# Kernel tuning notes

Hardware: AMD Instinct MI355X
Metric: run time of the kernel (lower is better)

Reference implementation:

```python
import jax, jax.numpy as jnp
import numpy as np

B, N, C, H = 1, 4096, 512, 8
S = 64  # sqrt(N), static


def setup_inputs() -> dict:
    key = jax.random.key(0)
    ks = jax.random.split(key, 4)
    d = C // H
    return {
        "x": jax.random.normal(ks[0], (B, N, C), dtype=jnp.float32),
        "num_heads": H,
        "bias": jnp.zeros((1,), dtype=jnp.float32),  # unused in original forward
        "scale": jnp.asarray(d ** -0.5, dtype=jnp.float32),
        "Wqkv": jax.random.normal(ks[1], (3 * C, C), dtype=jnp.float32) * (C ** -0.5),
        "bqkv": jnp.zeros((3 * C,), dtype=jnp.float32),
        "Wproj": jax.random.normal(ks[2], (C, C), dtype=jnp.float32) * (C ** -0.5),
        "bproj": jnp.zeros((C,), dtype=jnp.float32),
    }


def reference(x, num_heads, bias, scale, Wqkv, bqkv, Wproj, bproj):
    b, n, c = x.shape
    d = c // num_heads
    # fused QKV projection: [b, n, 3c] -> [3, b, h, n, d]
    qkv = (x @ Wqkv.T + bqkv).reshape(b, n, 3, num_heads, d).transpose(2, 0, 3, 1, 4)
    q, k, v = qkv[0] * scale, qkv[1], qkv[2]
    attn = jax.nn.softmax(jnp.einsum("bhnd,bhmd->bhnm", q, k), axis=-1)
    out = jnp.einsum("bhnm,bhmd->bhnd", attn, v)
    out = out.transpose(0, 2, 1, 3).reshape(b, n, c)
    out = out @ Wproj.T + bproj
    return out.reshape(b, S, S, c)
```

## Files before the change

kernel.cpp:

```cpp
#include <hip/hip_runtime.h>
#include <stdint.h>

#define NTOK 4096
#define CDIM 512
#define HEADS 8
#define DHEAD 64
#define PHEAD (NTOK * DHEAD)

typedef __bf16 bf16x8 __attribute__((ext_vector_type(8)));
typedef float f32x4 __attribute__((ext_vector_type(4)));

__device__ __forceinline__ unsigned short bfbits(float f) {
    return __builtin_bit_cast(unsigned short, (__bf16)f);
}

__device__ __forceinline__ f32x4 mfma32(bf16x8 a, bf16x8 b, f32x4 c) {
    return __builtin_amdgcn_mfma_f32_16x16x32_bf16(a, b, c, 0, 0, 0);
}

__device__ __forceinline__ void stage8(unsigned short* dst, const float* src) {
    const float4 v0 = *(const float4*)src;
    const float4 v1 = *(const float4*)(src + 4);
    ushort4 o0, o1;
    o0.x = bfbits(v0.x); o0.y = bfbits(v0.y); o0.z = bfbits(v0.z); o0.w = bfbits(v0.w);
    o1.x = bfbits(v1.x); o1.y = bfbits(v1.y); o1.z = bfbits(v1.z); o1.w = bfbits(v1.w);
    *(ushort4*)dst = o0;
    *(ushort4*)(dst + 4) = o1;
}

__global__ __launch_bounds__(256) void gemm_qkv(
    const float* __restrict__ A,
    const float* __restrict__ Bm,
    const float* __restrict__ bias,
    const float* __restrict__ scale_p,
    unsigned short* __restrict__ qkv_out)
{
    __shared__ __align__(16) unsigned short smem[64 * 136];
    unsigned short* lA = smem;
    unsigned short* lB = smem + 2048;

    const int tid = threadIdx.x;
    const int mBase = blockIdx.y * 64, nBase = blockIdx.x * 128;
    const int lane = tid & 63;
    const int w = __builtin_amdgcn_readfirstlane(tid >> 6);
    const int l16 = lane & 15, quad = lane >> 4;
    const int srow = tid >> 2, scol = (tid & 3) * 8;

    f32x4 acc[4][2] = {};

    for (int kt = 0; kt < CDIM; kt += 32) {
        __syncthreads();
        stage8(&lA[srow * 32 + scol], &A[(size_t)(mBase + srow) * CDIM + kt + scol]);
#pragma unroll
        for (int p = 0; p < 2; ++p) {
            const int r = p * 64 + srow;
            stage8(&lB[r * 32 + scol], &Bm[(size_t)(nBase + r) * CDIM + kt + scol]);
        }
        __syncthreads();

        bf16x8 af[4], bfr[2];
#pragma unroll
        for (int i = 0; i < 4; ++i)
            af[i] = *(const bf16x8*)&lA[(i * 16 + l16) * 32 + quad * 8];
#pragma unroll
        for (int j = 0; j < 2; ++j)
            bfr[j] = *(const bf16x8*)&lB[(w * 32 + j * 16 + l16) * 32 + quad * 8];
#pragma unroll
        for (int i = 0; i < 4; ++i)
#pragma unroll
            for (int j = 0; j < 2; ++j)
                acc[i][j] = mfma32(af[i], bfr[j], acc[i][j]);
    }

    const int three = nBase >> 9;
    const float scl = scale_p[0] * 1.44269504f;
    const float mul = (three == 0) ? scl : 1.0f;

    __syncthreads();
#pragma unroll
    for (int i = 0; i < 4; ++i)
#pragma unroll
        for (int j = 0; j < 2; ++j)
#pragma unroll
            for (int r = 0; r < 4; ++r) {
                const int rl = i * 16 + quad * 4 + r;
                const int cl = w * 32 + j * 16 + l16;
                const float v = (acc[i][j][r] + bias[nBase + cl]) * mul;
                smem[rl * 136 + cl] = bfbits(v);
            }
    __syncthreads();

    const size_t base3 = (size_t)three * (PHEAD * HEADS);
    if (three < 2) {
#pragma unroll
        for (int pass = 0; pass < 4; ++pass) {
            const int idx = pass * 256 + tid;
            const int rl16 = idx & 15, qc = (idx >> 4) & 7;
            const int hsel = (idx >> 7) & 1, t16l = (idx >> 8) & 3;
            const uint4 d = *(const uint4*)&smem[(t16l * 16 + rl16) * 136 + hsel * 64 + qc * 8];
            const int hh = ((nBase >> 6) + hsel) & 7;
            const int t16 = (mBase >> 4) + t16l;
            const size_t dst = base3 + (size_t)hh * PHEAD +
                (size_t)(((t16 * 2 + (qc >> 2)) * 64 + (qc & 3) * 16 + rl16) * 8);
            *(uint4*)&qkv_out[dst] = d;
        }
    } else {
#pragma unroll
        for (int pass = 0; pass < 4; ++pass) {
            const int idx = pass * 256 + tid;
            const int l16t = idx & 15, quadt = (idx >> 4) & 3;
            const int dt = (idx >> 6) & 3, k32l = (idx >> 8) & 1, hsel = (idx >> 9) & 1;
            const int col = hsel * 64 + dt * 16 + l16t;
            unsigned short o8[8];
#pragma unroll
            for (int e = 0; e < 4; ++e) {
                o8[e]     = smem[(k32l * 32 + quadt * 4 + e) * 136 + col];
                o8[e + 4] = smem[(k32l * 32 + 16 + quadt * 4 + e) * 136 + col];
            }
            const int hh = ((nBase >> 6) + hsel) & 7;
            const int k32 = (mBase >> 5) + k32l;
            const size_t dst = base3 + (size_t)hh * PHEAD +
                (size_t)(((k32 * 4 + dt) * 64 + quadt * 16 + l16t) * 8);
            *(uint4*)&qkv_out[dst] = *(uint4*)o8;
        }
    }
}

__global__ __launch_bounds__(256, 4) void flash6_k(
    const unsigned short* __restrict__ qf,
    const unsigned short* __restrict__ kf,
    const unsigned short* __restrict__ vf,
    unsigned short* __restrict__ attn_out)
{
    __shared__ float ldsO[4][32][68];
    __shared__ float sml[4][32];

    const int tid = threadIdx.x;
    const int lane = tid & 63;
    const int w = __builtin_amdgcn_readfirstlane(tid >> 6);
    const int l16 = lane & 15, quad = lane >> 4;
    const int h = blockIdx.x, qb = blockIdx.y;

    const unsigned short* qh = qf + (size_t)h * PHEAD;
    const unsigned short* kb = kf + (size_t)h * PHEAD + w * 65536;
    const unsigned short* vb = vf + (size_t)h * PHEAD + w * 65536;

    bf16x8 qfr[2][2];
#pragma unroll
    for (int qt = 0; qt < 2; ++qt)
#pragma unroll
        for (int d2 = 0; d2 < 2; ++d2)
            qfr[qt][d2] = *(const bf16x8*)&qh[((qb * 2 + qt) * 2 + d2) * 512 + lane * 8];

    bf16x8 ones;
#pragma unroll
    for (int j = 0; j < 8; ++j) ones[j] = (__bf16)1.0f;

    f32x4 oacc[4][2] = {};
    f32x4 lacc[2] = {};

    bf16x8 kA[4], kB[4];
#pragma unroll
    for (int i = 0; i < 4; ++i)
        kA[i] = *(const bf16x8*)&kb[i * 512 + lane * 8];

    auto body = [&](int g, bf16x8* kuse, bf16x8* kload) {
#pragma unroll
        for (int i = 0; i < 4; ++i)
            kload[i] = *(const bf16x8*)&kb[(g + 1) * 2048 + i * 512 + lane * 8];
        bf16x8 vc[4];
#pragma unroll
        for (int i = 0; i < 4; ++i)
            vc[i] = *(const bf16x8*)&vb[g * 2048 + i * 512 + lane * 8];

        f32x4 s[2][2];
#pragma unroll
        for (int kt = 0; kt < 2; ++kt)
#pragma unroll
            for (int qt = 0; qt < 2; ++qt) {
                f32x4 a = {};
                a = mfma32(kuse[kt * 2 + 0], qfr[qt][0], a);
                a = mfma32(kuse[kt * 2 + 1], qfr[qt][1], a);
                s[kt][qt] = a;
            }

        bf16x8 pf[2];
#pragma unroll
        for (int qt = 0; qt < 2; ++qt) {
            bf16x8 pb;
#pragma unroll
            for (int kt = 0; kt < 2; ++kt)
#pragma unroll
                for (int r = 0; r < 4; ++r)
                    pb[kt * 4 + r] = (__bf16)__builtin_amdgcn_exp2f(s[kt][qt][r]);
            pf[qt] = pb;
            lacc[qt] = mfma32(ones, pb, lacc[qt]);
        }
#pragma unroll
        for (int dt = 0; dt < 4; ++dt)
#pragma unroll
            for (int qt = 0; qt < 2; ++qt)
                oacc[dt][qt] = mfma32(vc[dt], pf[qt], oacc[dt][qt]);
    };

    for (int it = 0; it < 16; ++it) {
        body(it * 2 + 0, kA, kB);
        body(it * 2 + 1, kB, kA);
    }

    if (quad == 0) {
#pragma unroll
        for (int qt = 0; qt < 2; ++qt) sml[w][qt * 16 + l16] = lacc[qt][0];
    }
    __syncthreads();
#pragma unroll
    for (int qt = 0; qt < 2; ++qt) {
        const int q = qt * 16 + l16;
#pragma unroll
        for (int dt = 0; dt < 4; ++dt)
            *(f32x4*)&ldsO[w][q][dt * 16 + quad * 4] = oacc[dt][qt];
    }
    __syncthreads();
    {
        const int q = tid >> 3, dseg = (tid & 7) * 8;
        const float L = sml[0][q] + sml[1][q] + sml[2][q] + sml[3][q];
        const float inv = 1.f / L;
        unsigned short o8[8];
#pragma unroll
        for (int i = 0; i < 8; ++i) {
            const float v = ldsO[0][q][dseg + i] + ldsO[1][q][dseg + i] +
                            ldsO[2][q][dseg + i] + ldsO[3][q][dseg + i];
            o8[i] = bfbits(v * inv);
        }
        *(uint4*)&attn_out[(size_t)(qb * 32 + q) * CDIM + h * DHEAD + dseg] = *(uint4*)o8;
    }
}

__global__ __launch_bounds__(256) void gemm_proj(
    const unsigned short* __restrict__ A,
    const float* __restrict__ Bm,
    const float* __restrict__ bias,
    float* __restrict__ c_out)
{
    __shared__ __align__(16) unsigned short smem[2 * 64 * 32];
    unsigned short* lA = smem;
    unsigned short* lB = smem + 2048;

    const int tid = threadIdx.x;
    const int mBase = blockIdx.y * 64, nBase = blockIdx.x * 64;
    const int lane = tid & 63;
    const int w = __builtin_amdgcn_readfirstlane(tid >> 6);
    const int l16 = lane & 15, quad = lane >> 4;
    const int srow = tid >> 2, scol = (tid & 3) * 8;

    f32x4 acc[4] = {};

    for (int kt = 0; kt < CDIM; kt += 32) {
        __syncthreads();
        *(uint4*)&lA[srow * 32 + scol] =
            *(const uint4*)&A[(size_t)(mBase + srow) * CDIM + kt + scol];
        stage8(&lB[srow * 32 + scol], &Bm[(size_t)(nBase + srow) * CDIM + kt + scol]);
        __syncthreads();

        bf16x8 af[4], bfr;
#pragma unroll
        for (int i = 0; i < 4; ++i)
            af[i] = *(const bf16x8*)&lA[(i * 16 + l16) * 32 + quad * 8];
        bfr = *(const bf16x8*)&lB[(w * 16 + l16) * 32 + quad * 8];
#pragma unroll
        for (int i = 0; i < 4; ++i)
            acc[i] = mfma32(af[i], bfr, acc[i]);
    }

#pragma unroll
    for (int i = 0; i < 4; ++i)
#pragma unroll
        for (int r = 0; r < 4; ++r) {
            const int grow = mBase + i * 16 + quad * 4 + r;
            const int gcol = nBase + w * 16 + l16;
            c_out[(size_t)grow * CDIM + gcol] = acc[i][r] + bias[gcol];
        }
}

extern "C" void kernel_launch(void* const* d_in, const int* in_sizes, int n_in,
                              void* d_out, int out_size, void* d_ws, size_t ws_size,
                              hipStream_t stream) {
    const float* x       = (const float*)d_in[0];
    const float* scale_p = (const float*)d_in[3];
    const float* Wqkv    = (const float*)d_in[4];
    const float* bqkv    = (const float*)d_in[5];
    const float* Wproj   = (const float*)d_in[6];
    const float* bproj   = (const float*)d_in[7];
    float* out = (float*)d_out;

    char* ws = (char*)d_ws;
    const size_t OFF_QKV  = 0;
    const size_t OFF_ATTN = 12582912;
    const size_t NEEDED   = OFF_ATTN + 4194304;
    if (ws_size < NEEDED) return;

    unsigned short* qkvb  = (unsigned short*)(ws + OFF_QKV);
    unsigned short* attnb = (unsigned short*)(ws + OFF_ATTN);

    gemm_qkv<<<dim3(12, 64), 256, 0, stream>>>(x, Wqkv, bqkv, scale_p, qkvb);

    const unsigned short* qfr = qkvb;
    const unsigned short* kfr = qkvb + (size_t)PHEAD * HEADS;
    const unsigned short* vfr = qkvb + (size_t)2 * PHEAD * HEADS;
    flash6_k<<<dim3(8, 128), 256, 0, stream>>>(qfr, kfr, vfr, attnb);

    gemm_proj<<<dim3(8, 64), 256, 0, stream>>>(attnb, Wproj, bproj, out);
}
```

Baseline: 139.7 us.

## Split attention over key halves and merge partial outputs in projection GEMM

Adds a new attention kernel in which each block handles 64 queries against one half of the keys, instead of 32 queries against all keys. The four waves each take a quarter of that half, and partial outputs and row sums are reduced through LDS. The kernel writes unnormalized fp32 partial outputs and row sums for each key split. A new projection GEMM sums the two partials, normalizes by the combined row sum, converts to bf16 and runs the output projection. The aim is more reuse of each K/V load across queries and better parallelism, at the cost of extra fp32 workspace traffic. The old path is kept as a fallback when the workspace is too small.

```diff
diff --git a/kernel.cpp b/kernel.cpp
--- a/kernel.cpp
+++ b/kernel.cpp
@@ -126,6 +126,197 @@
     }
 }
 
+__global__ __launch_bounds__(256, 2) void flash7b_k(
+    const unsigned short* __restrict__ qf,
+    const unsigned short* __restrict__ kf,
+    const unsigned short* __restrict__ vf,
+    float* __restrict__ Opart,
+    float* __restrict__ lpart)
+{
+    __shared__ float ldsO[2][64][68];
+    __shared__ float sml[4][64];
+
+    const int tid = threadIdx.x;
+    const int lane = tid & 63;
+    const int w = __builtin_amdgcn_readfirstlane(tid >> 6);
+    const int l16 = lane & 15, quad = lane >> 4;
+    const int h = blockIdx.x, qb = blockIdx.y, ks = blockIdx.z;
+
+    const unsigned short* qh = qf + (size_t)h * PHEAD;
+    const unsigned short* kb = kf + (size_t)h * PHEAD + ks * 131072 + w * 32768;
+    const unsigned short* vb = vf + (size_t)h * PHEAD + ks * 131072 + w * 32768;
+
+    bf16x8 qfr[4][2];
+#pragma unroll
+    for (int qt = 0; qt < 4; ++qt)
+#pragma unroll
+        for (int d2 = 0; d2 < 2; ++d2)
+            qfr[qt][d2] = *(const bf16x8*)&qh[((qb * 4 + qt) * 2 + d2) * 512 + lane * 8];
+
+    bf16x8 ones;
+#pragma unroll
+    for (int j = 0; j < 8; ++j) ones[j] = (__bf16)1.0f;
+
+    f32x4 oacc[4][4] = {};
+    f32x4 lacc[4] = {};
+
+    bf16x8 kA[4], kB[4];
+#pragma unroll
+    for (int i = 0; i < 4; ++i)
+        kA[i] = *(const bf16x8*)&kb[i * 512 + lane * 8];
+
+    auto body = [&](int g, bf16x8* kuse, bf16x8* kload) {
+#pragma unroll
+        for (int i = 0; i < 4; ++i)
+            kload[i] = *(const bf16x8*)&kb[(g + 1) * 2048 + i * 512 + lane * 8];
+        bf16x8 vc[4];
+#pragma unroll
+        for (int i = 0; i < 4; ++i)
+            vc[i] = *(const bf16x8*)&vb[g * 2048 + i * 512 + lane * 8];
+
+        f32x4 s[2][4];
+#pragma unroll
+        for (int kt = 0; kt < 2; ++kt)
+#pragma unroll
+            for (int qt = 0; qt < 4; ++qt) {
+                f32x4 a = {};
+                a = mfma32(kuse[kt * 2 + 0], qfr[qt][0], a);
+                a = mfma32(kuse[kt * 2 + 1], qfr[qt][1], a);
+                s[kt][qt] = a;
+            }
+
+        bf16x8 pf[4];
+#pragma unroll
+        for (int qt = 0; qt < 4; ++qt) {
+            bf16x8 pb;
+#pragma unroll
+            for (int kt = 0; kt < 2; ++kt)
+#pragma unroll
+                for (int r = 0; r < 4; ++r)
+                    pb[kt * 4 + r] = (__bf16)__builtin_amdgcn_exp2f(s[kt][qt][r]);
+            pf[qt] = pb;
+            lacc[qt] = mfma32(ones, pb, lacc[qt]);
+        }
+#pragma unroll
+        for (int dt = 0; dt < 4; ++dt)
+#pragma unroll
+            for (int qt = 0; qt < 4; ++qt)
+                oacc[dt][qt] = mfma32(vc[dt], pf[qt], oacc[dt][qt]);
+    };
+
+    for (int it = 0; it < 8; ++it) {
+        body(it * 2 + 0, kA, kB);
+        body(it * 2 + 1, kB, kA);
+    }
+
+    if (w == 0 || w == 2) {
+        const int b = w >> 1;
+#pragma unroll
+        for (int qt = 0; qt < 4; ++qt)
+#pragma unroll
+            for (int dt = 0; dt < 4; ++dt)
+                *(f32x4*)&ldsO[b][qt * 16 + l16][dt * 16 + quad * 4] = oacc[dt][qt];
+    }
+    if (quad == 0) {
+#pragma unroll
+        for (int qt = 0; qt < 4; ++qt) sml[w][qt * 16 + l16] = lacc[qt][0];
+    }
+    __syncthreads();
+    if (w == 1 || w == 3) {
+        const int b = w >> 1;
+#pragma unroll
+        for (int qt = 0; qt < 4; ++qt)
+#pragma unroll
+            for (int dt = 0; dt < 4; ++dt) {
+                float* p = &ldsO[b][qt * 16 + l16][dt * 16 + quad * 4];
+                const f32x4 prev = *(const f32x4*)p;
+                *(f32x4*)p = prev + oacc[dt][qt];
+            }
+    }
+    __syncthreads();
+    {
+        const int q = tid >> 2, db = (tid & 3) * 16;
+        float* dst = &Opart[(size_t)ks * (NTOK * CDIM) +
+                            (size_t)(qb * 64 + q) * CDIM + h * DHEAD + db];
+#pragma unroll
+        for (int j4 = 0; j4 < 4; ++j4) {
+            f32x4 v;
+#pragma unroll
+            for (int e = 0; e < 4; ++e)
+                v[e] = ldsO[0][q][db + j4 * 4 + e] + ldsO[1][q][db + j4 * 4 + e];
+            *(f32x4*)(dst + j4 * 4) = v;
+        }
+        if (tid < 64) {
+            const float L = sml[0][tid] + sml[1][tid] + sml[2][tid] + sml[3][tid];
+            lpart[(size_t)ks * (HEADS * NTOK) + h * NTOK + qb * 64 + tid] = L;
+        }
+    }
+}
+
+__global__ __launch_bounds__(256) void gemm_proj_m(
+    const float* __restrict__ O0,
+    const float* __restrict__ O1,
+    const float* __restrict__ l0,
+    const float* __restrict__ l1,
+    const float* __restrict__ Bm,
+    const float* __restrict__ bias,
+    float* __restrict__ c_out)
+{
+    __shared__ __align__(16) unsigned short smem[2 * 64 * 32];
+    unsigned short* lA = smem;
+    unsigned short* lB = smem + 2048;
+
+    const int tid = threadIdx.x;
+    const int mBase = blockIdx.y * 64, nBase = blockIdx.x * 64;
+    const int lane = tid & 63;
+    const int w = __builtin_amdgcn_readfirstlane(tid >> 6);
+    const int l16 = lane & 15, quad = lane >> 4;
+    const int srow = tid >> 2, scol = (tid & 3) * 8;
+
+    f32x4 acc[4] = {};
+
+    for (int kt = 0; kt < CDIM; kt += 32) {
+        const int head = kt >> 6;
+        __syncthreads();
+        {
+            const int row = mBase + srow;
+            const float invl = __builtin_amdgcn_rcpf(
+                l0[head * NTOK + row] + l1[head * NTOK + row]);
+            const float4 a0 = *(const float4*)&O0[(size_t)row * CDIM + kt + scol];
+            const float4 b0 = *(const float4*)&O1[(size_t)row * CDIM + kt + scol];
+            const float4 a1 = *(const float4*)&O0[(size_t)row * CDIM + kt + scol + 4];
+            const float4 b1 = *(const float4*)&O1[(size_t)row * CDIM + kt + scol + 4];
+            ushort4 o0, o1;
+            o0.x = bfbits((a0.x + b0.x) * invl); o0.y = bfbits((a0.y + b0.y) * invl);
+            o0.z = bfbits((a0.z + b0.z) * invl); o0.w = bfbits((a0.w + b0.w) * invl);
+            o1.x = bfbits((a1.x + b1.x) * invl); o1.y = bfbits((a1.y + b1.y) * invl);
+            o1.z = bfbits((a1.z + b1.z) * invl); o1.w = bfbits((a1.w + b1.w) * invl);
+            *(ushort4*)&lA[srow * 32 + scol] = o0;
+            *(ushort4*)&lA[srow * 32 + scol + 4] = o1;
+        }
+        stage8(&lB[srow * 32 + scol], &Bm[(size_t)(nBase + srow) * CDIM + kt + scol]);
+        __syncthreads();
+
+        bf16x8 af[4], bfr;
+#pragma unroll
+        for (int i = 0; i < 4; ++i)
+            af[i] = *(const bf16x8*)&lA[(i * 16 + l16) * 32 + quad * 8];
+        bfr = *(const bf16x8*)&lB[(w * 16 + l16) * 32 + quad * 8];
+#pragma unroll
+        for (int i = 0; i < 4; ++i)
+            acc[i] = mfma32(af[i], bfr, acc[i]);
+    }
+
+#pragma unroll
+    for (int i = 0; i < 4; ++i)
+#pragma unroll
+        for (int r = 0; r < 4; ++r) {
+            const int grow = mBase + i * 16 + quad * 4 + r;
+            const int gcol = nBase + w * 16 + l16;
+            c_out[(size_t)grow * CDIM + gcol] = acc[i][r] + bias[gcol];
+        }
+}
+
 __global__ __launch_bounds__(256, 4) void flash6_k(
     const unsigned short* __restrict__ qf,
     const unsigned short* __restrict__ kf,
@@ -294,20 +485,32 @@
     float* out = (float*)d_out;
 
     char* ws = (char*)d_ws;
-    const size_t OFF_QKV  = 0;
-    const size_t OFF_ATTN = 12582912;
-    const size_t NEEDED   = OFF_ATTN + 4194304;
-    if (ws_size < NEEDED) return;
-
-    unsigned short* qkvb  = (unsigned short*)(ws + OFF_QKV);
-    unsigned short* attnb = (unsigned short*)(ws + OFF_ATTN);
+    const size_t OFF_QKV = 0;
+    const size_t OFF_O0  = 12582912;
+    const size_t OFF_O1  = OFF_O0 + 8388608;
+    const size_t OFF_L   = OFF_O1 + 8388608;
+    const size_t NEED_A  = OFF_L + 262144;
+    const size_t NEED_B  = 12582912 + 4194304;
+    if (ws_size < NEED_B) return;
+
+    unsigned short* qkvb = (unsigned short*)(ws + OFF_QKV);
 
     gemm_qkv<<<dim3(12, 64), 256, 0, stream>>>(x, Wqkv, bqkv, scale_p, qkvb);
 
     const unsigned short* qfr = qkvb;
     const unsigned short* kfr = qkvb + (size_t)PHEAD * HEADS;
     const unsigned short* vfr = qkvb + (size_t)2 * PHEAD * HEADS;
-    flash6_k<<<dim3(8, 128), 256, 0, stream>>>(qfr, kfr, vfr, attnb);
-
-    gemm_proj<<<dim3(8, 64), 256, 0, stream>>>(attnb, Wproj, bproj, out);
-}
+
+    if (ws_size >= NEED_A) {
+        float* O0 = (float*)(ws + OFF_O0);
+        float* O1 = (float*)(ws + OFF_O1);
+        float* l0 = (float*)(ws + OFF_L);
+        float* l1 = l0 + HEADS * NTOK;
+        flash7b_k<<<dim3(8, 64, 2), 256, 0, stream>>>(qfr, kfr, vfr, O0, l0);
+        gemm_proj_m<<<dim3(8, 64), 256, 0, stream>>>(O0, O1, l0, l1, Wproj, bproj, out);
+    } else {
+        unsigned short* attnb = (unsigned short*)(ws + OFF_O0);
+        flash6_k<<<dim3(8, 128), 256, 0, stream>>>(qfr, kfr, vfr, attnb);
+        gemm_proj<<<dim3(8, 64), 256, 0, stream>>>(attnb, Wproj, bproj, out);
+    }
+}
```

Result: slower. 162.7 us (+16.5%).
